# Optimization experiments

Hardware: AMD Instinct MI355X
Metric: run time of the kernel (lower is better)

## Reference

```python
import jax, jax.numpy as jnp
import numpy as np

HID = 1024      # hidden_size (embedding dim, GRU input)
RNN = 1024      # rnn_hidden_size
VOCAB = 50000   # max_node
STEPS = 1024    # num_steps
SOS = 0


def setup_inputs() -> dict:
    key = jax.random.key(0)
    ks = jax.random.split(key, 8)
    s = 0.02
    return {
        "inputs": jax.random.randint(ks[0], (STEPS,), 0, VOCAB),
        "z": jax.random.normal(ks[1], (RNN,), jnp.float32),
        "emb_W": jax.random.uniform(ks[2], (VOCAB, HID), jnp.float32, -0.001, 0.001),
        "out_b": jnp.full((VOCAB,), 0.01, jnp.float32),
        "h2e_W": jax.random.normal(ks[3], (HID, RNN), jnp.float32) * s,
        "h2e_b": jnp.full((HID,), 0.01, jnp.float32),
        "W_ih": jax.random.normal(ks[4], (3 * RNN, HID), jnp.float32) * s,
        "W_hh": jax.random.normal(ks[5], (3 * RNN, RNN), jnp.float32) * s,
        "b_ih": jnp.zeros((3 * RNN,), jnp.float32),
        "b_hh": jnp.zeros((3 * RNN,), jnp.float32),
    }


def reference(inputs, z, emb_W, out_b, h2e_W, h2e_b, W_ih, W_hh, b_ih, b_hh):
    R = RNN

    def gru_cell(h, x):
        gi = W_ih @ x + b_ih          # (3R,)
        gh = W_hh @ h + b_hh          # (3R,)
        r = jax.nn.sigmoid(gi[:R] + gh[:R])
        zg = jax.nn.sigmoid(gi[R:2 * R] + gh[R:2 * R])
        n = jnp.tanh(gi[2 * R:] + r * gh[2 * R:])
        return (1.0 - zg) * n + zg * h

    # teacher forcing: step i consumes token_{i-1} (SOS for i=1), target is inputs[i]
    step_tokens = jnp.concatenate([jnp.array([SOS], dtype=inputs.dtype), inputs[1:-1]])
    targets = inputs[1:]

    def step(h, tok_tgt):
        tok, tgt = tok_tgt
        x = emb_W[tok]                              # embedding lookup (HID,)
        h_new = gru_cell(h, x)                      # (RNN,)
        e = h2e_W @ h_new + h2e_b                   # (HID,)
        logp = jax.nn.log_softmax(emb_W @ e + out_b)  # tied weights, (VOCAB,)
        return h_new, (-logp[tgt], jnp.argmax(logp))

    _, (losses, preds) = jax.lax.scan(step, z, (step_tokens, targets))
    loss = jnp.sum(losses)
    outputs = jnp.zeros((1, inputs.shape[0]), dtype=jnp.int32).at[0, 1:].set(preds.astype(jnp.int32))
    return loss, outputs
```

## Files before the change

### kernel.cpp

```cpp
#include <hip/hip_runtime.h>
#include <math.h>

#define NV      50000
#define T_STEPS 1023
#define KDIM    1024
#define NCH     782
typedef unsigned long long ull;


__global__ __launch_bounds__(256) void k_gather(const int* __restrict__ inputs,
                                                const float* __restrict__ emb,
                                                float* __restrict__ X) {
  const int t = blockIdx.x;
  const int tid = threadIdx.x;
  float4 v = make_float4(0.f, 0.f, 0.f, 0.f);
  if (t < T_STEPS) {
    const int tok = (t == 0) ? 0 : inputs[t];
    v = *(const float4*)&emb[(size_t)tok * KDIM + tid * 4];
  }
  *(float4*)&X[(size_t)t * KDIM + tid * 4] = v;
}

__global__ __launch_bounds__(256) void k_initz(const float* __restrict__ z,
                                               double* __restrict__ Hm1) {
  const int i = blockIdx.x * 256 + threadIdx.x;
  Hm1[i] = (double)z[i];
}

__global__ __launch_bounds__(256) void k_gemm_ffd(const float* __restrict__ A,
                                                  const float* __restrict__ B,
                                                  const float* __restrict__ bias,
                                                  double* __restrict__ C,
                                                  int N, int K) {
  __shared__ float As[32][68];
  __shared__ float Bs[32][68];
  const int tid = threadIdx.x;
  const int bx = blockIdx.x, by = blockIdx.y;
  const int lr = tid >> 2;
  const int lk = (tid & 3) * 8;
  const float* Ap = A + (size_t)(by * 64 + lr) * K + lk;
  const float* Bp = B + (size_t)(bx * 64 + lr) * K + lk;
  const int r0 = (tid >> 4) * 4;
  const int c0 = (tid & 15) * 4;
  double acc[4][4] = {};
  for (int kc = 0; kc < K; kc += 32) {
    const float4 a0 = *(const float4*)(Ap + kc);
    const float4 a1 = *(const float4*)(Ap + kc + 4);
    const float4 b0 = *(const float4*)(Bp + kc);
    const float4 b1 = *(const float4*)(Bp + kc + 4);
    __syncthreads();
    As[lk+0][lr]=a0.x; As[lk+1][lr]=a0.y; As[lk+2][lr]=a0.z; As[lk+3][lr]=a0.w;
    As[lk+4][lr]=a1.x; As[lk+5][lr]=a1.y; As[lk+6][lr]=a1.z; As[lk+7][lr]=a1.w;
    Bs[lk+0][lr]=b0.x; Bs[lk+1][lr]=b0.y; Bs[lk+2][lr]=b0.z; Bs[lk+3][lr]=b0.w;
    Bs[lk+4][lr]=b1.x; Bs[lk+5][lr]=b1.y; Bs[lk+6][lr]=b1.z; Bs[lk+7][lr]=b1.w;
    __syncthreads();
#pragma unroll
    for (int kk = 0; kk < 32; ++kk) {
      const float4 av = *(const float4*)&As[kk][r0];
      const float4 bv = *(const float4*)&Bs[kk][c0];
      const double aa[4] = {av.x, av.y, av.z, av.w};
      const double bb[4] = {bv.x, bv.y, bv.z, bv.w};
#pragma unroll
      for (int i = 0; i < 4; ++i)
#pragma unroll
        for (int j = 0; j < 4; ++j)
          acc[i][j] = fma(aa[i], bb[j], acc[i][j]);
    }
  }
  const int row = by * 64 + r0;
  const int col = bx * 64 + c0;
#pragma unroll
  for (int i = 0; i < 4; ++i)
#pragma unroll
    for (int j = 0; j < 4; ++j)
      C[(size_t)(row + i) * N + col + j] = acc[i][j] + (double)bias[col + j];
}

__global__ __launch_bounds__(256) void k_gemm_dfd(const double* __restrict__ A,
                                                  const float* __restrict__ B,
                                                  const float* __restrict__ bias,
                                                  double* __restrict__ C,
                                                  int N, int K) {
  __shared__ double As[32][68];
  __shared__ float  Bs[32][68];
  const int tid = threadIdx.x;
  const int bx = blockIdx.x, by = blockIdx.y;
  const int lr = tid >> 2;
  const int lk = (tid & 3) * 8;
  const double* Ap = A + (size_t)(by * 64 + lr) * K + lk;
  const float*  Bp = B + (size_t)(bx * 64 + lr) * K + lk;
  const int r0 = (tid >> 4) * 4;
  const int c0 = (tid & 15) * 4;
  double acc[4][4] = {};
  for (int kc = 0; kc < K; kc += 32) {
    double ar[8];
#pragma unroll
    for (int q = 0; q < 8; ++q) ar[q] = Ap[kc + q];
    const float4 b0 = *(const float4*)(Bp + kc);
    const float4 b1 = *(const float4*)(Bp + kc + 4);
    __syncthreads();
#pragma unroll
    for (int q = 0; q < 8; ++q) As[lk + q][lr] = ar[q];
    Bs[lk+0][lr]=b0.x; Bs[lk+1][lr]=b0.y; Bs[lk+2][lr]=b0.z; Bs[lk+3][lr]=b0.w;
    Bs[lk+4][lr]=b1.x; Bs[lk+5][lr]=b1.y; Bs[lk+6][lr]=b1.z; Bs[lk+7][lr]=b1.w;
    __syncthreads();
#pragma unroll
    for (int kk = 0; kk < 32; ++kk) {
      const double aa[4] = {As[kk][r0+0], As[kk][r0+1], As[kk][r0+2], As[kk][r0+3]};
      const float4 bv = *(const float4*)&Bs[kk][c0];
      const double bb[4] = {bv.x, bv.y, bv.z, bv.w};
#pragma unroll
      for (int i = 0; i < 4; ++i)
#pragma unroll
        for (int j = 0; j < 4; ++j)
          acc[i][j] = fma(aa[i], bb[j], acc[i][j]);
    }
  }
  const int row = by * 64 + r0;
  const int col = bx * 64 + c0;
#pragma unroll
  for (int i = 0; i < 4; ++i)
#pragma unroll
    for (int j = 0; j < 4; ++j)
      C[(size_t)(row + i) * N + col + j] = acc[i][j] + (double)bias[col + j];
}

__global__ __launch_bounds__(512) void k_step(const float* __restrict__ Whh,
                                              const float* __restrict__ bhh,
                                              const double* __restrict__ gi_row,
                                              const double* __restrict__ h_prev,
                                              double* __restrict__ h_out) {
  __shared__ double hs[1024];
  const int tid = threadIdx.x;
  const int w = tid >> 6, l = tid & 63;
  const int i = blockIdx.x * 8 + w;
  hs[tid]       = h_prev[tid];
  hs[tid + 512] = h_prev[tid + 512];
  __syncthreads();
  const float* w_r = Whh + (size_t)i * 1024;
  const float* w_z = Whh + (size_t)(1024 + i) * 1024;
  const float* w_n = Whh + (size_t)(2048 + i) * 1024;
  double sr = 0.0, sz = 0.0, sn = 0.0;
#pragma unroll 4
  for (int m = 0; m < 16; ++m) {
    const int k = l + 64 * m;
    const double hv = hs[k];
    sr = fma((double)w_r[k], hv, sr);
    sz = fma((double)w_z[k], hv, sz);
    sn = fma((double)w_n[k], hv, sn);
  }
#pragma unroll
  for (int mk = 32; mk >= 1; mk >>= 1) {
    sr += __shfl_xor(sr, mk, 64);
    sz += __shfl_xor(sz, mk, 64);
    sn += __shfl_xor(sn, mk, 64);
  }
  if (l == 0) {
    const double r  = 1.0 / (1.0 + exp(-(gi_row[i]        + sr + (double)bhh[i])));
    const double zg = 1.0 / (1.0 + exp(-(gi_row[1024 + i] + sz + (double)bhh[1024 + i])));
    const double n  = tanh(gi_row[2048 + i] + r * (sn + (double)bhh[2048 + i]));
    h_out[i] = (1.0 - zg) * n + zg * hs[i];
  }
}

__global__ __launch_bounds__(256) void k_logits(const double* __restrict__ E,
                                                const float* __restrict__ emb,
                                                const float* __restrict__ out_b,
                                                const int* __restrict__ inputs,
                                                float* __restrict__ candL,
                                                int* __restrict__ candI,
                                                float* __restrict__ Psum,
                                                float* __restrict__ Ttgt) {
  __shared__ double As[32][68];
  __shared__ float  Bs[32][68];
  const int tid = threadIdx.x;
  const int bx = blockIdx.x, by = blockIdx.y;
  const int lr = tid >> 2;
  const int lk = (tid & 3) * 8;
  const int brow = bx * 64 + lr;
  const double* Ap = E + (size_t)(by * 64 + lr) * KDIM + lk;
  const float*  Bp = emb + (size_t)brow * KDIM + lk;
  const bool bvalid = (brow < NV);
  const int r0 = (tid >> 4) * 4;
  const int c0 = (tid & 15) * 4;
  double acc[4][4] = {};
  for (int kc = 0; kc < KDIM; kc += 32) {
    double ar[8];
#pragma unroll
    for (int q = 0; q < 8; ++q) ar[q] = Ap[kc + q];
    float4 b0 = make_float4(0.f, 0.f, 0.f, 0.f);
    float4 b1 = make_float4(0.f, 0.f, 0.f, 0.f);
    if (bvalid) { b0 = *(const float4*)(Bp + kc); b1 = *(const float4*)(Bp + kc + 4); }
    __syncthreads();
#pragma unroll
    for (int q = 0; q < 8; ++q) As[lk + q][lr] = ar[q];
    Bs[lk+0][lr]=b0.x; Bs[lk+1][lr]=b0.y; Bs[lk+2][lr]=b0.z; Bs[lk+3][lr]=b0.w;
    Bs[lk+4][lr]=b1.x; Bs[lk+5][lr]=b1.y; Bs[lk+6][lr]=b1.z; Bs[lk+7][lr]=b1.w;
    __syncthreads();
#pragma unroll
    for (int kk = 0; kk < 32; ++kk) {
      const double aa[4] = {As[kk][r0+0], As[kk][r0+1], As[kk][r0+2], As[kk][r0+3]};
      const float4 bv = *(const float4*)&Bs[kk][c0];
      const double bb[4] = {bv.x, bv.y, bv.z, bv.w};
#pragma unroll
      for (int i = 0; i < 4; ++i)
#pragma unroll
        for (int j = 0; j < 4; ++j)
          acc[i][j] = fma(aa[i], bb[j], acc[i][j]);
    }
  }
  const int colb = bx * 64 + c0;
#pragma unroll
  for (int i = 0; i < 4; ++i) {
    const int s = by * 64 + r0 + i;
    const bool valid = (s < T_STEPS);
    const int tgt = valid ? inputs[s + 1] : -1;
    float L1 = -3e38f, L2 = -3e38f;
    int   i1 = 0x7FFFFFFF, i2 = 0x7FFFFFFF;
    float se = 0.f, tv = -INFINITY;
#pragma unroll
    for (int j = 0; j < 4; ++j) {
      const int v = colb + j;
      if (v < NV) {
        const double lgd = acc[i][j] + (double)out_b[v];
        const float L = (float)lgd;
        se += expf((float)(lgd - 0.01));
        if (v == tgt) tv = (float)lgd;
        if (L > L1 || (L == L1 && v < i1)) { L2 = L1; i2 = i1; L1 = L; i1 = v; }
        else if (L > L2 || (L == L2 && v < i2)) { L2 = L; i2 = v; }
      }
    }
#pragma unroll
    for (int mk = 1; mk <= 8; mk <<= 1) {
      const float oL1 = __shfl_xor(L1, mk, 64); const int oi1 = __shfl_xor(i1, mk, 64);
      const float oL2 = __shfl_xor(L2, mk, 64); const int oi2 = __shfl_xor(i2, mk, 64);
      if (oL1 > L1 || (oL1 == L1 && oi1 < i1)) { L2 = L1; i2 = i1; L1 = oL1; i1 = oi1; }
      else if (oL1 > L2 || (oL1 == L2 && oi1 < i2)) { L2 = oL1; i2 = oi1; }
      if (oL2 > L1 || (oL2 == L1 && oi2 < i1)) { L2 = L1; i2 = i1; L1 = oL2; i1 = oi2; }
      else if (oL2 > L2 || (oL2 == L2 && oi2 < i2)) { L2 = oL2; i2 = oi2; }
      se += __shfl_xor(se, mk, 64);
      tv = fmaxf(tv, __shfl_xor(tv, mk, 64));
    }
    if (((tid & 15) == 0) && valid) {
      const size_t p = (size_t)s * (2 * NCH) + 2 * bx;
      candL[p] = L1;     candI[p] = i1;
      candL[p + 1] = L2; candI[p + 1] = i2;
      atomicAdd(&Psum[s], se);
      if (tv > -1e30f) Ttgt[s] = tv;
    }
  }
}

__global__ __launch_bounds__(256) void k_preds(const float* __restrict__ candL,
                                               const int* __restrict__ candI,
                                               float* __restrict__ out) {
  __shared__ float sL[256];
  __shared__ int   sI[256];
  const int s = blockIdx.x;
  const int tid = threadIdx.x;
  const int n = 2 * NCH;
  const size_t base = (size_t)s * n;
  float m = -3e38f;
  for (int c = tid; c < n; c += 256) m = fmaxf(m, candL[base + c]);
  sL[tid] = m; __syncthreads();
  for (int st = 128; st > 0; st >>= 1) {
    if (tid < st) sL[tid] = fmaxf(sL[tid], sL[tid + st]);
    __syncthreads();
  }
  const float Lmax = sL[0];
  __syncthreads();
  float bq = -3e38f; int bi = 0x7FFFFFFF;
  for (int c = tid; c < n; c += 256) {
    const float L = candL[base + c];
    const int   v = candI[base + c];
    const float d = L - Lmax;
    const float q = d - 10.8125f;
    if (q > bq || (q == bq && v < bi)) { bq = q; bi = v; }
  }
  sL[tid] = bq; sI[tid] = bi; __syncthreads();
  for (int st = 128; st > 0; st >>= 1) {
    if (tid < st) {
      if (sL[tid + st] > sL[tid] ||
          (sL[tid + st] == sL[tid] && sI[tid + st] < sI[tid])) {
        sL[tid] = sL[tid + st]; sI[tid] = sI[tid + st];
      }
    }
    __syncthreads();
  }
  if (tid == 0) out[2 + s] = (float)sI[0];
}

__global__ __launch_bounds__(1024) void k_finish(const float* __restrict__ Psum,
                                                 const float* __restrict__ Ttgt,
                                                 float* __restrict__ out) {
  __shared__ double red[1024];
  const int s = threadIdx.x;
  double ls = 0.0;
  if (s < T_STEPS) ls = 0.01 + log((double)Psum[s]) - (double)Ttgt[s];
  red[s] = ls;
  __syncthreads();
  for (int st = 512; st > 0; st >>= 1) {
    if (s < st) red[s] += red[s + st];
    __syncthreads();
  }
  if (s == 0) out[0] = (float)red[0];
  if (s == 1) out[1] = 0.f;
}

extern "C" void kernel_launch(void* const* d_in, const int* in_sizes, int n_in,
                              void* d_out, int out_size, void* d_ws, size_t ws_size,
                              hipStream_t stream) {
  const int*   inputs = (const int*)  d_in[0];
  const float* z      = (const float*)d_in[1];
  const float* emb    = (const float*)d_in[2];
  const float* out_b  = (const float*)d_in[3];
  const float* h2eW   = (const float*)d_in[4];
  const float* h2eb   = (const float*)d_in[5];
  const float* Wih    = (const float*)d_in[6];
  const float* Whh    = (const float*)d_in[7];
  const float* bih    = (const float*)d_in[8];
  const float* bhh    = (const float*)d_in[9];

  char* ws8 = (char*)d_ws;
  float*  Psum = (float*)(ws8 + 8192);
  float*  Ttgt = (float*)(ws8 + 12288);
  double* Hm1  = (double*)(ws8 + 16384);
  float*  X    = (float*)(ws8 + 24576);
  char*   GIb  = ws8 + 24576 + (4u << 20);
  double* GI   = (double*)GIb;
  double* E    = GI;
  float*  candL = (float*)(GIb + (8u << 20));
  int*    candI = (int*)  (GIb + (8u << 20) + 6815744);
  double* H    = (double*)(ws8 + 24576 + (28u << 20));
  float*  out  = (float*)d_out;

  hipMemsetAsync(ws8, 0, 16384, stream);

  k_gather<<<1024, 256, 0, stream>>>(inputs, emb, X);
  k_initz<<<4, 256, 0, stream>>>(z, Hm1);
  k_gemm_ffd<<<dim3(48, 16), 256, 0, stream>>>(X, Wih, bih, GI, 3072, KDIM);

  for (int t = 0; t < T_STEPS; ++t) {
    const double* hp = (t == 0) ? Hm1 : (H + (size_t)(t - 1) * KDIM);
    k_step<<<128, 512, 0, stream>>>(Whh, bhh, GI + (size_t)t * 3072,
                                    hp, H + (size_t)t * KDIM);
  }

  k_gemm_dfd<<<dim3(16, 16), 256, 0, stream>>>(H, h2eW, h2eb, E, KDIM, KDIM);
  k_logits<<<dim3(NCH, 16), 256, 0, stream>>>(E, emb, out_b, inputs,
                                              candL, candI, Psum, Ttgt);
  k_preds<<<T_STEPS, 256, 0, stream>>>(candL, candI, out);
  k_finish<<<1, 1024, 0, stream>>>(Psum, Ttgt, out);
}
```

Measured before the change: 10.50 ms.

## Replace per-step GRU launches with persistent kernel using grid-wide atomic barrier

The 1023 separate recurrence launches become one persistent kernel of 64 blocks. Each block keeps its slice of W_hh in registers across all steps and moves between steps through a global atomic counter barrier. This removes per-step launch overhead and the repeated W_hh reload from memory. The cost is a grid-wide spin barrier whose correctness depends on all 64 blocks being resident at once, plus heavy register pressure from holding 96 floats of weights per thread.

Measured after the change: 14.79 ms. 40.8% more time.

```diff
diff --git a/kernel.cpp b/kernel.cpp
--- a/kernel.cpp
+++ b/kernel.cpp
@@ -19,12 +19,6 @@
     v = *(const float4*)&emb[(size_t)tok * KDIM + tid * 4];
   }
   *(float4*)&X[(size_t)t * KDIM + tid * 4] = v;
-}
-
-__global__ __launch_bounds__(256) void k_initz(const float* __restrict__ z,
-                                               double* __restrict__ Hm1) {
-  const int i = blockIdx.x * 256 + threadIdx.x;
-  Hm1[i] = (double)z[i];
 }
 
 __global__ __launch_bounds__(256) void k_gemm_ffd(const float* __restrict__ A,
@@ -125,41 +119,82 @@
       C[(size_t)(row + i) * N + col + j] = acc[i][j] + (double)bias[col + j];
 }
 
-__global__ __launch_bounds__(512) void k_step(const float* __restrict__ Whh,
-                                              const float* __restrict__ bhh,
-                                              const double* __restrict__ gi_row,
-                                              const double* __restrict__ h_prev,
-                                              double* __restrict__ h_out) {
+__global__ __launch_bounds__(512, 2) void k_recur(const float* __restrict__ z,
+                                                  const float* __restrict__ Whh,
+                                                  const float* __restrict__ bhh,
+                                                  const double* __restrict__ GI,
+                                                  double* H, int* cnt) {
   __shared__ double hs[1024];
   const int tid = threadIdx.x;
   const int w = tid >> 6, l = tid & 63;
-  const int i = blockIdx.x * 8 + w;
-  hs[tid]       = h_prev[tid];
-  hs[tid + 512] = h_prev[tid + 512];
-  __syncthreads();
-  const float* w_r = Whh + (size_t)i * 1024;
-  const float* w_z = Whh + (size_t)(1024 + i) * 1024;
-  const float* w_n = Whh + (size_t)(2048 + i) * 1024;
-  double sr = 0.0, sz = 0.0, sn = 0.0;
-#pragma unroll 4
-  for (int m = 0; m < 16; ++m) {
-    const int k = l + 64 * m;
-    const double hv = hs[k];
-    sr = fma((double)w_r[k], hv, sr);
-    sz = fma((double)w_z[k], hv, sz);
-    sn = fma((double)w_n[k], hv, sn);
-  }
-#pragma unroll
-  for (int mk = 32; mk >= 1; mk >>= 1) {
-    sr += __shfl_xor(sr, mk, 64);
-    sz += __shfl_xor(sz, mk, 64);
-    sn += __shfl_xor(sn, mk, 64);
-  }
-  if (l == 0) {
-    const double r  = 1.0 / (1.0 + exp(-(gi_row[i]        + sr + (double)bhh[i])));
-    const double zg = 1.0 / (1.0 + exp(-(gi_row[1024 + i] + sz + (double)bhh[1024 + i])));
-    const double n  = tanh(gi_row[2048 + i] + r * (sn + (double)bhh[2048 + i]));
-    h_out[i] = (1.0 - zg) * n + zg * hs[i];
+  const int ibase = blockIdx.x * 16 + w * 2;
+  float wreg[6][16];
+#pragma unroll
+  for (int il = 0; il < 2; ++il)
+#pragma unroll
+    for (int g = 0; g < 3; ++g) {
+      const float* wp = Whh + (size_t)(g * 1024 + ibase + il) * 1024 + l;
+#pragma unroll
+      for (int m = 0; m < 16; ++m) wreg[il * 3 + g][m] = wp[m * 64];
+    }
+  double bh[6];
+#pragma unroll
+  for (int il = 0; il < 2; ++il)
+#pragma unroll
+    for (int g = 0; g < 3; ++g) bh[il * 3 + g] = (double)bhh[g * 1024 + ibase + il];
+
+  for (int t = 0; t < T_STEPS; ++t) {
+    if (t == 0) {
+      hs[tid]       = (double)z[tid];
+      hs[tid + 512] = (double)z[tid + 512];
+    } else {
+      const double* hp = H + (size_t)(t - 1) * 1024;
+      hs[tid]       = __hip_atomic_load(hp + tid,
+                        __ATOMIC_RELAXED, __HIP_MEMORY_SCOPE_AGENT);
+      hs[tid + 512] = __hip_atomic_load(hp + tid + 512,
+                        __ATOMIC_RELAXED, __HIP_MEMORY_SCOPE_AGENT);
+    }
+    __syncthreads();
+    double gi[6];
+    {
+      const double* gp = GI + (size_t)t * 3072;
+#pragma unroll
+      for (int il = 0; il < 2; ++il)
+#pragma unroll
+        for (int g = 0; g < 3; ++g) gi[il * 3 + g] = gp[g * 1024 + ibase + il];
+    }
+    double s[6] = {0.0, 0.0, 0.0, 0.0, 0.0, 0.0};
+#pragma unroll
+    for (int m = 0; m < 16; ++m) {
+      const double hv = hs[l + 64 * m];
+#pragma unroll
+      for (int rr = 0; rr < 6; ++rr) s[rr] = fma((double)wreg[rr][m], hv, s[rr]);
+    }
+#pragma unroll
+    for (int rr = 0; rr < 6; ++rr) {
+      double v = s[rr];
+#pragma unroll
+      for (int mk = 32; mk >= 1; mk >>= 1) v += __shfl_xor(v, mk, 64);
+      s[rr] = v;
+    }
+    if (l < 2) {
+      const int il = l;
+      const double r  = 1.0 / (1.0 + exp(-(gi[il * 3 + 0] + s[il * 3 + 0] + bh[il * 3 + 0])));
+      const double zg = 1.0 / (1.0 + exp(-(gi[il * 3 + 1] + s[il * 3 + 1] + bh[il * 3 + 1])));
+      const double n  = tanh(gi[il * 3 + 2] + r * (s[il * 3 + 2] + bh[il * 3 + 2]));
+      const int gidx = ibase + il;
+      const double hn = (1.0 - zg) * n + zg * hs[gidx];
+      __hip_atomic_store(H + (size_t)t * 1024 + gidx, hn,
+                         __ATOMIC_RELAXED, __HIP_MEMORY_SCOPE_AGENT);
+    }
+    __syncthreads();
+    if (tid == 0) {
+      __hip_atomic_fetch_add(cnt, 1, __ATOMIC_RELEASE, __HIP_MEMORY_SCOPE_AGENT);
+      const int target = (t + 1) * 64;
+      while (__hip_atomic_load(cnt, __ATOMIC_ACQUIRE, __HIP_MEMORY_SCOPE_AGENT) < target)
+        __builtin_amdgcn_s_sleep(1);
+    }
+    __syncthreads();
   }
 }
 
@@ -322,9 +357,9 @@
   const float* bhh    = (const float*)d_in[9];
 
   char* ws8 = (char*)d_ws;
+  int*    cnt  = (int*)ws8;
   float*  Psum = (float*)(ws8 + 8192);
   float*  Ttgt = (float*)(ws8 + 12288);
-  double* Hm1  = (double*)(ws8 + 16384);
   float*  X    = (float*)(ws8 + 24576);
   char*   GIb  = ws8 + 24576 + (4u << 20);
   double* GI   = (double*)GIb;
@@ -337,15 +372,8 @@
   hipMemsetAsync(ws8, 0, 16384, stream);
 
   k_gather<<<1024, 256, 0, stream>>>(inputs, emb, X);
-  k_initz<<<4, 256, 0, stream>>>(z, Hm1);
   k_gemm_ffd<<<dim3(48, 16), 256, 0, stream>>>(X, Wih, bih, GI, 3072, KDIM);
-
-  for (int t = 0; t < T_STEPS; ++t) {
-    const double* hp = (t == 0) ? Hm1 : (H + (size_t)(t - 1) * KDIM);
-    k_step<<<128, 512, 0, stream>>>(Whh, bhh, GI + (size_t)t * 3072,
-                                    hp, H + (size_t)t * KDIM);
-  }
-
+  k_recur<<<64, 512, 0, stream>>>(z, Whh, bhh, GI, H, cnt);
   k_gemm_dfd<<<dim3(16, 16), 256, 0, stream>>>(H, h2eW, h2eb, E, KDIM, KDIM);
   k_logits<<<dim3(NCH, 16), 256, 0, stream>>>(E, emb, out_b, inputs,
                                               candL, candI, Psum, Ttgt);
```
